# Performance work log

Measured on AMD Instinct MI355X. Metric: run time of the kernel, lower is better.

The kernel has to match this reference:

```python
import jax, jax.numpy as jnp
import numpy as np

N = 100000   # nodes
E = 1600000  # edges
IN = 128     # input_dim
H = 64       # hidden_dim
OUT = 2      # output_dim
G = 64       # number of graphs in the batch


def setup_inputs() -> dict:
    key = jax.random.key(0)
    ks = jax.random.split(key, 12)
    x = jax.random.normal(ks[0], (N, IN), dtype=jnp.float32)
    edge_index = jax.random.randint(ks[1], (2, E), 0, N, dtype=jnp.int64)
    batch = jnp.sort(jax.random.randint(ks[2], (N,), 0, G, dtype=jnp.int64))
    s = 0.05
    return {
        "x": x,
        "edge_index": edge_index,
        "batch": batch,
        "W1": jax.random.normal(ks[3], (IN, H), dtype=jnp.float32) * s,
        "b1": jnp.zeros((H,), dtype=jnp.float32),
        "W2": jax.random.normal(ks[4], (H, H), dtype=jnp.float32) * s,
        "b2": jnp.zeros((H,), dtype=jnp.float32),
        "W3": jax.random.normal(ks[5], (H, H), dtype=jnp.float32) * s,
        "b3": jnp.zeros((H,), dtype=jnp.float32),
        "Wm1": jax.random.normal(ks[6], (H, H), dtype=jnp.float32) * s,
        "bm1": jnp.zeros((H,), dtype=jnp.float32),
        "Wm2": jax.random.normal(ks[7], (H, OUT), dtype=jnpp.float32) * s if False else jax.random.normal(ks[7], (H, OUT), dtype=jnp.float32) * s,
        "bm2": jnp.zeros((OUT,), dtype=jnp.float32),
    }


def _gcn_conv(x, W, b, src, dst, norm, n_nodes):
    # PyG GCNConv: h = x @ W; message = norm * h[src]; scatter-add at dst; + bias
    h = x @ W                                  # [N, H]
    msg = h[src] * norm[:, None]               # [E+N, H] gather + scale
    out = jax.ops.segment_sum(msg, dst, num_segments=n_nodes)
    return out + b


def reference(x, edge_index, batch, W1, b1, W2, b2, W3, b3, Wm1, bm1, Wm2, bm2):
    n = x.shape[0]
    # add self-loops (PyG GCNConv default add_self_loops=True)
    loop = jnp.arange(n, dtype=edge_index.dtype)
    src = jnp.concatenate([edge_index[0], loop])
    dst = jnp.concatenate([edge_index[1], loop])
    # symmetric normalization deg^-1/2 (deg over target nodes, incl. self-loops)
    deg = jax.ops.segment_sum(jnp.ones_like(dst, dtype=x.dtype), dst, num_segments=n)
    dinv = jnp.where(deg > 0, jax.lax.rsqrt(deg), 0.0)
    norm = dinv[src] * dinv[dst]               # [E+N]

    h = jax.nn.relu(_gcn_conv(x, W1, b1, src, dst, norm, n))   # dropout: eval -> identity
    h = jax.nn.relu(_gcn_conv(h, W2, b2, src, dst, norm, n))
    h = jax.nn.relu(_gcn_conv(h, W3, b3, src, dst, norm, n))

    # global_mean_pool over batch ids
    sums = jax.ops.segment_sum(h, batch, num_segments=G)       # [G, H]
    cnts = jax.ops.segment_sum(jnp.ones((n,), dtype=h.dtype), batch, num_segments=G)
    pooled = sums / jnp.maximum(cnts, 1.0)[:, None]

    # MLP head: Linear -> ReLU -> (Dropout eval) -> Linear
    z = jax.nn.relu(pooled @ Wm1 + bm1)
    return z @ Wm2 + bm2                                       # [G, OUT]
```

## Files before the change

kernel.cpp:

```cpp
#include <hip/hip_runtime.h>
#include <hip/hip_bf16.h>

#define NNODES 100000
#define NEDGES 1600000
#define IND 128
#define HD 64
#define OUTD 2
#define NG 64
#define SCAN_CHUNK 1024
#define BINSHIFT 9
#define BINSZ 512
#define PB 256

typedef __attribute__((ext_vector_type(8))) short short8v;
typedef __attribute__((ext_vector_type(4))) float floatx4;

static __device__ __forceinline__ unsigned short f2bf(float f) {
    __hip_bfloat16 h = __float2bfloat16(f);
    return *(unsigned short*)&h;
}
static __device__ __forceinline__ float bf2f(unsigned short u) {
    __hip_bfloat16 h = *(__hip_bfloat16*)&u;
    return __bfloat162float(h);
}

__global__ __launch_bounds__(256) void binA_kernel(const int* __restrict__ dst,
                                                   int* __restrict__ bbc,
                                                   int E, int nbins) {
    __shared__ int lh[256];
    lh[threadIdx.x] = 0;
    __syncthreads();
    int ebpb = (E + PB - 1) / PB;
    int e0 = blockIdx.x * ebpb;
    int e1 = min(e0 + ebpb, E);
    for (int e = e0 + threadIdx.x; e < e1; e += 256)
        atomicAdd(&lh[dst[e] >> BINSHIFT], 1);
    __syncthreads();
    bbc[blockIdx.x * 256 + threadIdx.x] = lh[threadIdx.x];
}

__global__ __launch_bounds__(256) void binB1_kernel(int* __restrict__ bbc,
                                                    int* __restrict__ binTotal,
                                                    int* __restrict__ binStart) {
    __shared__ int ws[4];
    int b = blockIdx.x;
    int t = threadIdx.x, lane = t & 63, wv = t >> 6;
    int v = bbc[t * 256 + b];
    int sc = v;
#pragma unroll
    for (int d = 1; d < 64; d <<= 1) { int u = __shfl_up(sc, d, 64); if (lane >= d) sc += u; }
    if (lane == 63) ws[wv] = sc;
    __syncthreads();
    int add = 0;
    for (int w = 0; w < wv; w++) add += ws[w];
    bbc[t * 256 + b] = sc - v + add;
    if (t == 255) { int tot = sc + add; binTotal[b] = tot; binStart[b] = tot; }
}

__global__ __launch_bounds__(64) void scan_bsums_kernel(int* __restrict__ bsum, int nchunks) {
    int lane = threadIdx.x;
    int cpl = (nchunks + 63) / 64;
    int vals[8];
    int i0 = lane * cpl;
    int t = 0;
    for (int k = 0; k < cpl; k++) {
        int i = i0 + k;
        vals[k] = (i < nchunks) ? bsum[i] : 0;
        t += vals[k];
    }
    int sc = t;
#pragma unroll
    for (int d = 1; d < 64; d <<= 1) { int v = __shfl_up(sc, d, 64); if (lane >= d) sc += v; }
    int ex = sc - t;
    for (int k = 0; k < cpl; k++) {
        int i = i0 + k;
        if (i < nchunks) bsum[i] = ex;
        ex += vals[k];
    }
}

__global__ __launch_bounds__(256) void binC_kernel(const int* __restrict__ src,
                                                   const int* __restrict__ dst,
                                                   const int* __restrict__ bbc,
                                                   const int* __restrict__ binStart,
                                                   unsigned int* __restrict__ binned,
                                                   int E, int nbins) {
    __shared__ int cur[256];
    int t = threadIdx.x;
    if (t < nbins) cur[t] = binStart[t] + bbc[blockIdx.x * 256 + t];
    __syncthreads();
    int ebpb = (E + PB - 1) / PB;
    int e0 = blockIdx.x * ebpb;
    int e1 = min(e0 + ebpb, E);
    for (int e = e0 + t; e < e1; e += 256) {
        int d = dst[e];
        int b = d >> BINSHIFT;
        int p = atomicAdd(&cur[b], 1);
        binned[p] = ((unsigned int)(d & (BINSZ - 1)) << 17) | (unsigned int)src[e];
    }
}

__global__ __launch_bounds__(256) void binH_kernel(const unsigned int* __restrict__ binned,
                                                   const int* __restrict__ binStart,
                                                   const int* __restrict__ binTotal,
                                                   int* __restrict__ hist,
                                                   float* __restrict__ dinv, int n) {
    __shared__ int dh[BINSZ];
    int b = blockIdx.x;
    int t = threadIdx.x;
    dh[t] = 0; dh[t + 256] = 0;
    __syncthreads();
    int s0 = binStart[b], cnt = binTotal[b];
    for (int i = t; i < cnt; i += 256)
        atomicAdd(&dh[binned[s0 + i] >> 17], 1);
    __syncthreads();
#pragma unroll
    for (int r = 0; r < 2; r++) {
        int i = t + r * 256;
        int node = (b << BINSHIFT) + i;
        if (node < n) {
            int dg = dh[i];
            hist[node] = dg;
            dinv[node] = 1.0f / sqrtf((float)(dg + 1));
        }
    }
}

__global__ __launch_bounds__(256) void scan_sum_kernel(const int* __restrict__ hist,
                                                       int* __restrict__ bsum, int n) {
    __shared__ int wsums[4];
    int lane = threadIdx.x & 63, wv = threadIdx.x >> 6;
    int i0 = blockIdx.x * SCAN_CHUNK + threadIdx.x * 4;
    int t = 0;
#pragma unroll
    for (int k = 0; k < 4; k++) { int i = i0 + k; if (i < n) t += hist[i]; }
#pragma unroll
    for (int d = 32; d > 0; d >>= 1) t += __shfl_down(t, d, 64);
    if (lane == 0) wsums[wv] = t;
    __syncthreads();
    if (threadIdx.x == 0) bsum[blockIdx.x] = wsums[0] + wsums[1] + wsums[2] + wsums[3];
}

__global__ __launch_bounds__(256) void scan_write_kernel(const int* __restrict__ hist,
                                                         const int* __restrict__ bofs,
                                                         int* __restrict__ rowptr,
                                                         int n, int total) {
    __shared__ int wsum[4];
    int lane = threadIdx.x & 63, wv = threadIdx.x >> 6;
    int i0 = blockIdx.x * SCAN_CHUNK + threadIdx.x * 4;
    int h[4]; int t = 0;
#pragma unroll
    for (int k = 0; k < 4; k++) { int i = i0 + k; h[k] = (i < n) ? hist[i] : 0; t += h[k]; }
    int sc = t;
#pragma unroll
    for (int d = 1; d < 64; d <<= 1) { int v = __shfl_up(sc, d, 64); if (lane >= d) sc += v; }
    if (lane == 63) wsum[wv] = sc;
    __syncthreads();
    int wofs = 0;
    for (int w = 0; w < wv; w++) wofs += wsum[w];
    int ex = (sc - t) + wofs + bofs[blockIdx.x];
#pragma unroll
    for (int k = 0; k < 4; k++) { int i = i0 + k; if (i < n) rowptr[i] = ex; ex += h[k]; }
    if (blockIdx.x == 0 && threadIdx.x == 0) rowptr[n] = total;
}

__global__ __launch_bounds__(256) void binD_kernel(const unsigned int* __restrict__ binned,
                                                   const int* __restrict__ binStart,
                                                   const int* __restrict__ binTotal,
                                                   const int* __restrict__ hist,
                                                   const int* __restrict__ rowptr,
                                                   int* __restrict__ ssrc, int n) {
    __shared__ int cntL[BINSZ];
    __shared__ int rpL[BINSZ];
    int b = blockIdx.x;
    int t = threadIdx.x;
#pragma unroll
    for (int r = 0; r < 2; r++) {
        int i = t + r * 256;
        int node = (b << BINSHIFT) + i;
        if (node < n) { cntL[i] = hist[node]; rpL[i] = rowptr[node]; }
    }
    __syncthreads();
    int s0 = binStart[b], cnt = binTotal[b];
    for (int i = t; i < cnt; i += 256) {
        unsigned int rec = binned[s0 + i];
        int doff = rec >> 17;
        int s = rec & 0x1FFFF;
        int idx = atomicSub(&cntL[doff], 1) - 1;
        ssrc[rpL[doff] + idx] = s;
    }
}

__global__ __launch_bounds__(256) void cvtWT_kernel(const float* __restrict__ W,
                                                    unsigned short* __restrict__ WT, int K) {
    int i = blockIdx.x * 256 + threadIdx.x;
    if (i < 64 * K) {
        int n = i / K, k = i - n * K;
        WT[i] = f2bf(W[k * 64 + n]);
    }
}

template <int K, bool BF16IN>
__global__ __launch_bounds__(256) void mm_mfma_kernel(const void* __restrict__ Xv,
                                                      const unsigned short* __restrict__ WT,
                                                      unsigned short* __restrict__ Tb, int nn) {
    const int lane = threadIdx.x & 63;
    const int wv   = threadIdx.x >> 6;
    const int nb   = blockIdx.x * 64 + wv * 16;
    if (nb >= nn) return;
    const int col  = lane & 15;
    const int quad = lane >> 4;
    const int m    = min(nb + col, nn - 1);

    floatx4 acc0 = {0.f, 0.f, 0.f, 0.f};
    floatx4 acc1 = {0.f, 0.f, 0.f, 0.f};
    floatx4 acc2 = {0.f, 0.f, 0.f, 0.f};
    floatx4 acc3 = {0.f, 0.f, 0.f, 0.f};

#pragma unroll
    for (int ks = 0; ks < K; ks += 32) {
        const int k0 = ks + quad * 8;
        short8v a;
        if (BF16IN) {
            a = *(const short8v*)((const unsigned short*)Xv + (size_t)m * K + k0);
        } else {
            const float* xr = (const float*)Xv + (size_t)m * K + k0;
            float4 f0 = *(const float4*)(xr);
            float4 f1 = *(const float4*)(xr + 4);
            a[0] = (short)f2bf(f0.x); a[1] = (short)f2bf(f0.y);
            a[2] = (short)f2bf(f0.z); a[3] = (short)f2bf(f0.w);
            a[4] = (short)f2bf(f1.x); a[5] = (short)f2bf(f1.y);
            a[6] = (short)f2bf(f1.z); a[7] = (short)f2bf(f1.w);
        }
        short8v b0 = *(const short8v*)(WT + (size_t)(0  + col) * K + k0);
        short8v b1 = *(const short8v*)(WT + (size_t)(16 + col) * K + k0);
        short8v b2 = *(const short8v*)(WT + (size_t)(32 + col) * K + k0);
        short8v b3 = *(const short8v*)(WT + (size_t)(48 + col) * K + k0);
        acc0 = __builtin_amdgcn_mfma_f32_16x16x32_bf16(a, b0, acc0, 0, 0, 0);
        acc1 = __builtin_amdgcn_mfma_f32_16x16x32_bf16(a, b1, acc1, 0, 0, 0);
        acc2 = __builtin_amdgcn_mfma_f32_16x16x32_bf16(a, b2, acc2, 0, 0, 0);
        acc3 = __builtin_amdgcn_mfma_f32_16x16x32_bf16(a, b3, acc3, 0, 0, 0);
    }

#pragma unroll
    for (int r = 0; r < 4; r++) {
        int node = nb + quad * 4 + r;
        if (node < nn) {
            unsigned short* o = Tb + (size_t)node * 64 + col;
            o[0]  = f2bf(acc0[r]);
            o[16] = f2bf(acc1[r]);
            o[32] = f2bf(acc2[r]);
            o[48] = f2bf(acc3[r]);
        }
    }
}

__global__ __launch_bounds__(256) void agg_kernel(const unsigned short* __restrict__ Tb,
                                                  const int* __restrict__ rowptr,
                                                  const int* __restrict__ ssrc,
                                                  const float* __restrict__ dinv,
                                                  const float* __restrict__ bias,
                                                  unsigned short* __restrict__ Ob, int nn) {
    int wave = __builtin_amdgcn_readfirstlane((blockIdx.x * 256 + threadIdx.x) >> 6);
    int lane = threadIdx.x & 63;
    if (wave >= nn) return;
    int n = wave;
    float di = dinv[n];
    float acc = di * di * bf2f(Tb[(size_t)n * 64 + lane]);
    int rb = rowptr[n], re = rowptr[n + 1];
    int i = rb;
    for (; i + 3 < re; i += 4) {
        int s0 = ssrc[i], s1 = ssrc[i + 1], s2 = ssrc[i + 2], s3 = ssrc[i + 3];
        float w0 = di * dinv[s0];
        float w1 = di * dinv[s1];
        float w2 = di * dinv[s2];
        float w3 = di * dinv[s3];
        float v0 = bf2f(Tb[(size_t)s0 * 64 + lane]);
        float v1 = bf2f(Tb[(size_t)s1 * 64 + lane]);
        float v2 = bf2f(Tb[(size_t)s2 * 64 + lane]);
        float v3 = bf2f(Tb[(size_t)s3 * 64 + lane]);
        acc += w0 * v0;
        acc += w1 * v1;
        acc += w2 * v2;
        acc += w3 * v3;
    }
    for (; i < re; i++) {
        int s0 = ssrc[i];
        acc += di * dinv[s0] * bf2f(Tb[(size_t)s0 * 64 + lane]);
    }
    float v = acc + bias[lane];
    Ob[(size_t)n * 64 + lane] = f2bf(v > 0.f ? v : 0.f);
}

__global__ __launch_bounds__(256) void pool_kernel(const unsigned short* __restrict__ Hb,
                                                   const int* __restrict__ batch,
                                                   float* __restrict__ pooled,
                                                   float* __restrict__ gcnt, int nn) {
    int wid = (blockIdx.x * 256 + threadIdx.x) >> 6;
    int lane = threadIdx.x & 63;
    int nwaves = (gridDim.x * 256) >> 6;
    int per = (nn + nwaves - 1) / nwaves;
    int n0 = wid * per;
    int n1 = n0 + per; if (n1 > nn) n1 = nn;
    if (n0 >= n1) return;
    int cur = batch[n0];
    float acc = 0.f, cnt = 0.f;
    for (int n = n0; n < n1; ++n) {
        int g = batch[n];
        if (g != cur) {
            atomicAdd(&pooled[cur * 64 + lane], acc);
            if (lane == 0) atomicAdd(&gcnt[cur], cnt);
            acc = 0.f; cnt = 0.f; cur = g;
        }
        acc += bf2f(Hb[(size_t)n * 64 + lane]);
        cnt += 1.f;
    }
    atomicAdd(&pooled[cur * 64 + lane], acc);
    if (lane == 0) atomicAdd(&gcnt[cur], cnt);
}

__global__ __launch_bounds__(256) void head_kernel(const float* __restrict__ pooled,
                                                   const float* __restrict__ gcnt,
                                                   const float* __restrict__ Wm1,
                                                   const float* __restrict__ bm1,
                                                   const float* __restrict__ Wm2,
                                                   const float* __restrict__ bm2,
                                                   float* __restrict__ out) {
    __shared__ float P[NG * 64];
    __shared__ float Z[NG * 64];
    int tid = threadIdx.x;
    for (int i = tid; i < NG * 64; i += 256) {
        int g = i >> 6;
        float c = gcnt[g];
        c = c > 1.f ? c : 1.f;
        P[i] = pooled[i] / c;
    }
    __syncthreads();
    for (int i = tid; i < NG * 64; i += 256) {
        int g = i >> 6, j = i & 63;
        float a = bm1[j];
#pragma unroll 8
        for (int k = 0; k < 64; ++k) a += P[g * 64 + k] * Wm1[k * 64 + j];
        Z[i] = a > 0.f ? a : 0.f;
    }
    __syncthreads();
    for (int i = tid; i < NG * OUTD; i += 256) {
        int g = i / OUTD, o = i % OUTD;
        float a = bm2[o];
#pragma unroll 8
        for (int k = 0; k < 64; ++k) a += Z[g * 64 + k] * Wm2[k * OUTD + o];
        out[i] = a;
    }
}

extern "C" void kernel_launch(void* const* d_in, const int* in_sizes, int n_in,
                              void* d_out, int out_size, void* d_ws, size_t ws_size,
                              hipStream_t stream) {
    const float* x    = (const float*)d_in[0];
    const int*  edge  = (const int*)d_in[1];
    const int*  batch = (const int*)d_in[2];
    const float* W1 = (const float*)d_in[3];
    const float* b1 = (const float*)d_in[4];
    const float* W2 = (const float*)d_in[5];
    const float* b2 = (const float*)d_in[6];
    const float* W3 = (const float*)d_in[7];
    const float* b3 = (const float*)d_in[8];
    const float* Wm1 = (const float*)d_in[9];
    const float* bm1 = (const float*)d_in[10];
    const float* Wm2 = (const float*)d_in[11];
    const float* bm2 = (const float*)d_in[12];

    const int N_ = in_sizes[2];
    const int E_ = in_sizes[1] / 2;
    const int* src = edge;
    const int* dst = edge + E_;
    const int nbins = (N_ + BINSZ - 1) >> BINSHIFT;

    char* w = (char*)d_ws;
    auto alloc = [&](size_t bytes) -> void* {
        void* p = (void*)w;
        w += (bytes + 255) & ~(size_t)255;
        return p;
    };
    float* dinv   = (float*)alloc((size_t)N_ * 4);
    int*   hist   = (int*)alloc((size_t)N_ * 4);
    int*   rowptr = (int*)alloc((size_t)(N_ + 1) * 4);
    int*   bsum   = (int*)alloc(512 * 4);
    int*   bbc    = (int*)alloc((size_t)256 * 256 * 4);
    int*   binTotal = (int*)alloc(256 * 4);
    int*   binStart = (int*)alloc(256 * 4);
    int*   ssrc   = (int*)alloc((size_t)E_ * 4);
    unsigned int* binned = (unsigned int*)alloc((size_t)E_ * 4);
    unsigned short* Tb  = (unsigned short*)alloc((size_t)N_ * 64 * 2);
    unsigned short* hBb = (unsigned short*)alloc((size_t)N_ * 64 * 2);
    unsigned short* WT1 = (unsigned short*)alloc((size_t)64 * IND * 2);
    unsigned short* WT2 = (unsigned short*)alloc((size_t)64 * HD * 2);
    unsigned short* WT3 = (unsigned short*)alloc((size_t)64 * HD * 2);
    float* pooled = (float*)alloc((size_t)(NG * 64 + NG) * 4);
    float* gcnt   = pooled + NG * 64;

    const int nchunks = (N_ + SCAN_CHUNK - 1) / SCAN_CHUNK;

    hipMemsetAsync(pooled, 0, (size_t)(NG * 64 + NG) * 4, stream);

    binA_kernel<<<PB, 256, 0, stream>>>(dst, bbc, E_, nbins);
    binB1_kernel<<<nbins, 256, 0, stream>>>(bbc, binTotal, binStart);
    scan_bsums_kernel<<<1, 64, 0, stream>>>(binStart, nbins);
    binC_kernel<<<PB, 256, 0, stream>>>(src, dst, bbc, binStart, binned, E_, nbins);
    binH_kernel<<<nbins, 256, 0, stream>>>(binned, binStart, binTotal, hist, dinv, N_);
    scan_sum_kernel<<<nchunks, 256, 0, stream>>>(hist, bsum, N_);
    scan_bsums_kernel<<<1, 64, 0, stream>>>(bsum, nchunks);
    scan_write_kernel<<<nchunks, 256, 0, stream>>>(hist, bsum, rowptr, N_, E_);
    binD_kernel<<<nbins, 256, 0, stream>>>(binned, binStart, binTotal, hist, rowptr, ssrc, N_);

    cvtWT_kernel<<<(64 * IND + 255) / 256, 256, 0, stream>>>(W1, WT1, IND);
    cvtWT_kernel<<<(64 * HD + 255) / 256, 256, 0, stream>>>(W2, WT2, HD);
    cvtWT_kernel<<<(64 * HD + 255) / 256, 256, 0, stream>>>(W3, WT3, HD);

    const int mmblk = (N_ + 63) / 64;
    const int aggblk = (N_ + 3) / 4;

    mm_mfma_kernel<IND, false><<<mmblk, 256, 0, stream>>>(x, WT1, Tb, N_);
    agg_kernel<<<aggblk, 256, 0, stream>>>(Tb, rowptr, ssrc, dinv, b1, hBb, N_);
    mm_mfma_kernel<HD, true><<<mmblk, 256, 0, stream>>>(hBb, WT2, Tb, N_);
    agg_kernel<<<aggblk, 256, 0, stream>>>(Tb, rowptr, ssrc, dinv, b2, hBb, N_);
    mm_mfma_kernel<HD, true><<<mmblk, 256, 0, stream>>>(hBb, WT3, Tb, N_);
    agg_kernel<<<aggblk, 256, 0, stream>>>(Tb, rowptr, ssrc, dinv, b3, hBb, N_);

    pool_kernel<<<256, 256, 0, stream>>>(hBb, batch, pooled, gcnt, N_);
    head_kernel<<<1, 256, 0, stream>>>(pooled, gcnt, Wm1, bm1, Wm2, bm2, (float*)d_out);
}
```

Baseline: 455.8 us.

## Prescale transformed features by dinv and split edges across quads in aggregation

The GEMM epilogue now multiplies each output row by dinv[node], so aggregation no longer needs a per-edge gather of dinv[src] and only scales the final sum by dinv[dst]. The aggregation kernel is restructured so each wave handles four edges at once: each 16-lane quad loads a full 64-feature row with ushort4 vector loads, and the quads are then reduced with cross-lane shuffles. This cuts per-edge random loads and raises memory-level parallelism. The trade-offs are extra shuffle reductions and idle quads on the final store, and rounding to bf16 now happens after the dinv scaling, which slightly changes numerics.

```diff
diff --git a/kernel.cpp b/kernel.cpp
--- a/kernel.cpp
+++ b/kernel.cpp
@@ -203,6 +203,7 @@
 template <int K, bool BF16IN>
 __global__ __launch_bounds__(256) void mm_mfma_kernel(const void* __restrict__ Xv,
                                                       const unsigned short* __restrict__ WT,
+                                                      const float* __restrict__ dinv,
                                                       unsigned short* __restrict__ Tb, int nn) {
     const int lane = threadIdx.x & 63;
     const int wv   = threadIdx.x >> 6;
@@ -246,11 +247,12 @@
     for (int r = 0; r < 4; r++) {
         int node = nb + quad * 4 + r;
         if (node < nn) {
+            float sc = dinv[node];
             unsigned short* o = Tb + (size_t)node * 64 + col;
-            o[0]  = f2bf(acc0[r]);
-            o[16] = f2bf(acc1[r]);
-            o[32] = f2bf(acc2[r]);
-            o[48] = f2bf(acc3[r]);
+            o[0]  = f2bf(sc * acc0[r]);
+            o[16] = f2bf(sc * acc1[r]);
+            o[32] = f2bf(sc * acc2[r]);
+            o[48] = f2bf(sc * acc3[r]);
         }
     }
 }
@@ -265,31 +267,39 @@
     int lane = threadIdx.x & 63;
     if (wave >= nn) return;
     int n = wave;
+    int quad = lane >> 4;
+    int fg = lane & 15;
+    int rb = rowptr[n], re = rowptr[n + 1];
+    float a0 = 0.f, a1 = 0.f, a2 = 0.f, a3 = 0.f;
+    for (int i = rb + quad; i < re; i += 4) {
+        int s = ssrc[i];
+        ushort4 v = *(const ushort4*)(Tb + (size_t)s * 64 + fg * 4);
+        a0 += bf2f(v.x);
+        a1 += bf2f(v.y);
+        a2 += bf2f(v.z);
+        a3 += bf2f(v.w);
+    }
+    a0 += __shfl_xor(a0, 16, 64); a0 += __shfl_xor(a0, 32, 64);
+    a1 += __shfl_xor(a1, 16, 64); a1 += __shfl_xor(a1, 32, 64);
+    a2 += __shfl_xor(a2, 16, 64); a2 += __shfl_xor(a2, 32, 64);
+    a3 += __shfl_xor(a3, 16, 64); a3 += __shfl_xor(a3, 32, 64);
+    ushort4 sv = *(const ushort4*)(Tb + (size_t)n * 64 + fg * 4);
+    a0 += bf2f(sv.x); a1 += bf2f(sv.y); a2 += bf2f(sv.z); a3 += bf2f(sv.w);
     float di = dinv[n];
-    float acc = di * di * bf2f(Tb[(size_t)n * 64 + lane]);
-    int rb = rowptr[n], re = rowptr[n + 1];
-    int i = rb;
-    for (; i + 3 < re; i += 4) {
-        int s0 = ssrc[i], s1 = ssrc[i + 1], s2 = ssrc[i + 2], s3 = ssrc[i + 3];
-        float w0 = di * dinv[s0];
-        float w1 = di * dinv[s1];
-        float w2 = di * dinv[s2];
-        float w3 = di * dinv[s3];
-        float v0 = bf2f(Tb[(size_t)s0 * 64 + lane]);
-        float v1 = bf2f(Tb[(size_t)s1 * 64 + lane]);
-        float v2 = bf2f(Tb[(size_t)s2 * 64 + lane]);
-        float v3 = bf2f(Tb[(size_t)s3 * 64 + lane]);
-        acc += w0 * v0;
-        acc += w1 * v1;
-        acc += w2 * v2;
-        acc += w3 * v3;
-    }
-    for (; i < re; i++) {
-        int s0 = ssrc[i];
-        acc += di * dinv[s0] * bf2f(Tb[(size_t)s0 * 64 + lane]);
-    }
-    float v = acc + bias[lane];
-    Ob[(size_t)n * 64 + lane] = f2bf(v > 0.f ? v : 0.f);
+    float4 bs = *(const float4*)(bias + fg * 4);
+    float o0 = di * a0 + bs.x;
+    float o1 = di * a1 + bs.y;
+    float o2 = di * a2 + bs.z;
+    float o3 = di * a3 + bs.w;
+    o0 = o0 > 0.f ? o0 : 0.f;
+    o1 = o1 > 0.f ? o1 : 0.f;
+    o2 = o2 > 0.f ? o2 : 0.f;
+    o3 = o3 > 0.f ? o3 : 0.f;
+    if (quad == 0) {
+        ushort4 p;
+        p.x = f2bf(o0); p.y = f2bf(o1); p.z = f2bf(o2); p.w = f2bf(o3);
+        *(ushort4*)(Ob + (size_t)n * 64 + fg * 4) = p;
+    }
 }
 
 __global__ __launch_bounds__(256) void pool_kernel(const unsigned short* __restrict__ Hb,
@@ -420,11 +430,11 @@
     const int mmblk = (N_ + 63) / 64;
     const int aggblk = (N_ + 3) / 4;
 
-    mm_mfma_kernel<IND, false><<<mmblk, 256, 0, stream>>>(x, WT1, Tb, N_);
+    mm_mfma_kernel<IND, false><<<mmblk, 256, 0, stream>>>(x, WT1, dinv, Tb, N_);
     agg_kernel<<<aggblk, 256, 0, stream>>>(Tb, rowptr, ssrc, dinv, b1, hBb, N_);
-    mm_mfma_kernel<HD, true><<<mmblk, 256, 0, stream>>>(hBb, WT2, Tb, N_);
+    mm_mfma_kernel<HD, true><<<mmblk, 256, 0, stream>>>(hBb, WT2, dinv, Tb, N_);
     agg_kernel<<<aggblk, 256, 0, stream>>>(Tb, rowptr, ssrc, dinv, b2, hBb, N_);
-    mm_mfma_kernel<HD, true><<<mmblk, 256, 0, stream>>>(hBb, WT3, Tb, N_);
+    mm_mfma_kernel<HD, true><<<mmblk, 256, 0, stream>>>(hBb, WT3, dinv, Tb, N_);
     agg_kernel<<<aggblk, 256, 0, stream>>>(Tb, rowptr, ssrc, dinv, b3, hBb, N_);
 
     pool_kernel<<<256, 256, 0, stream>>>(hBb, batch, pooled, gcnt, N_);
```

After: 456.6 us. No clear change (+0.2%).
